# Optimization experiments

Hardware: AMD Instinct MI355X
Metric: run time of the kernel (lower is better)

Reference implementation:

```python
import jax, jax.numpy as jnp
import numpy as np

GROUP_SIZE = 128
EQN = "btd,kdf->btkf"  # x:[B,T,D] @ w:[K,D,F] -> [B,T,K,F]


def setup_inputs() -> dict:
    key = jax.random.key(0)
    k1, k2, k3, k4 = jax.random.split(key, 4)
    B, T, D = 4, 2048, 4096
    K, F = 2, 8192
    G = D // GROUP_SIZE  # 32 quantization groups along D
    x = jax.random.normal(k1, (B, T, D), dtype=jnp.float32)
    qweight = jax.random.randint(k2, (K, D, F), 0, 16, dtype=jnp.int32)  # uint4 values
    qzeros = jax.random.randint(k3, (K, G, F), 0, 16, dtype=jnp.int32)   # uint4 zero points
    scales = jax.random.uniform(k4, (K, G, F), dtype=jnp.float32) * 0.02
    return {"x": x, "qweight": qweight, "qzeros": qzeros, "scales": scales}


def dequantize(imatrix, scales, zeros, group_size, axis_to_repeat):
    rs = jnp.repeat(scales, group_size, axis=axis_to_repeat)
    rz = jnp.repeat(zeros, group_size, axis=axis_to_repeat)
    return (imatrix.astype(rs.dtype) - rz.astype(rs.dtype)) * rs


def reference(x, qweight, qzeros, scales):
    # dequantize int4 weights along axis 1 (hidden/contraction dim), then einsum
    w = dequantize(qweight, scales, qzeros, GROUP_SIZE, axis_to_repeat=1)  # [K,D,F] fp32
    w = w.astype(x.dtype)
    return jnp.einsum(EQN, x, w)  # [B,T,K,F]
```

## Files before the change

kernel.cpp:

```cpp
#include <hip/hip_runtime.h>
#include <hip/hip_bf16.h>
#include <stdint.h>


typedef __attribute__((ext_vector_type(8))) short bf16x8;
typedef __attribute__((ext_vector_type(16))) float f32x16;
typedef __attribute__((ext_vector_type(4))) float f32x4;

static constexpr int Dd = 4096, Ff = 8192;
static constexpr int M = 8192, NTOT = 16384;
static constexpr int NKT2 = Dd / 32;
static constexpr int NMB = M / 256;
static constexpr int NNB = NTOT / 256;

__device__ __forceinline__ short f2bf(float f) {
    __hip_bfloat16 h = __float2bfloat16(f);
    return *reinterpret_cast<short*>(&h);
}

__device__ __forceinline__ int frag_off32(int r, int cb) {
    const int rb = r >> 5, ks = cb >> 1, kh = cb & 1;
    return ((rb * 2 + ks) << 10) + (((r & 31) + 32 * kh) << 4);
}

__global__ __launch_bounds__(256) void xcvt(const float* __restrict__ x,
                                            char* __restrict__ Xw) {
    const int bid = blockIdx.x;
    const int h = bid >> 7, kt2 = bid & 127;
    const int t = threadIdx.x;
    const int r = t >> 1, seg = t & 1;
    const float* src = x + ((size_t)(h * 128 + r)) * Dd + kt2 * 32 + seg * 16;
    char* panel = Xw + ((size_t)bid << 13);
    #pragma unroll
    for (int jj = 0; jj < 2; ++jj) {
        float4 v0 = *reinterpret_cast<const float4*>(src + jj * 8);
        float4 v1 = *reinterpret_cast<const float4*>(src + jj * 8 + 4);
        union { short s[8]; bf16x8 v; } u;
        u.s[0] = f2bf(v0.x); u.s[1] = f2bf(v0.y); u.s[2] = f2bf(v0.z); u.s[3] = f2bf(v0.w);
        u.s[4] = f2bf(v1.x); u.s[5] = f2bf(v1.y); u.s[6] = f2bf(v1.z); u.s[7] = f2bf(v1.w);
        const int cb = seg * 2 + jj;
        *reinterpret_cast<bf16x8*>(panel + frag_off32(r, cb)) = u.v;
    }
}

__global__ __launch_bounds__(256) void wdq(const int* __restrict__ qw,
                                           const int* __restrict__ qz,
                                           const float* __restrict__ sc,
                                           char* __restrict__ Ww) {
    const int bid = blockIdx.x;
    const int fh = bid >> 7, kt2 = bid & 127;
    const int t = threadIdx.x;
    const int r = t & 127, dh = t >> 7;
    const int n = fh * 128 + r;
    const int k = n >> 13, f = n & 8191;
    const int g = kt2 >> 2;
    const int   zv = qz[((size_t)k * 32 + g) * Ff + f];
    const float sv = sc[((size_t)k * 32 + g) * Ff + f];
    const int* qp = qw + ((size_t)(k * Dd + kt2 * 32 + dh * 16)) * Ff + f;
    char* panel = Ww + ((size_t)bid << 13);
    #pragma unroll
    for (int jj = 0; jj < 2; ++jj) {
        union { short s[8]; bf16x8 v; } u;
        #pragma unroll
        for (int e = 0; e < 8; ++e) {
            int q = qp[(size_t)(jj * 8 + e) * Ff];
            u.s[e] = f2bf((float)(q - zv) * sv);
        }
        const int cb = dh * 2 + jj;
        *reinterpret_cast<bf16x8*>(panel + frag_off32(r, cb)) = u.v;
    }
}

#define APAN32(H, KT2) (Xw + (((size_t)(H) * 128 + (KT2)) << 13))
#define BPAN32(H, KT2) (Ww + (((size_t)(H) * 128 + (KT2)) << 13))

#define GLL(GP, LP)                                                                \
    __builtin_amdgcn_global_load_lds(                                              \
        (const __attribute__((address_space(1))) void*)(GP),                       \
        (__attribute__((address_space(3))) void*)(LP), 16, 0, 0)

#define STAGE_TILE(KT2, BUF) do {                                                  \
    GLL(APAN32(bm2,     (KT2)) + woff16, (BUF) +     0 + woffu);                   \
    GLL(APAN32(bm2 + 1, (KT2)) + woff16, (BUF) +  8192 + woffu);                   \
    GLL(BPAN32(bn2,     (KT2)) + woff16, (BUF) + 16384 + woffu);                   \
    GLL(BPAN32(bn2 + 1, (KT2)) + woff16, (BUF) + 24576 + woffu);                   \
} while (0)

#define SB0() __builtin_amdgcn_sched_barrier(0)

#define BODY(KT2, BUFR, DOST, BUFS) do {                                           \
    if (DOST) STAGE_TILE((KT2) + 2, BUFS);                                         \
    bf16x8 a[8], b[4];                                                             \
    _Pragma("unroll")                                                              \
    for (int mb = 0; mb < 4; ++mb)                                                 \
        _Pragma("unroll")                                                          \
        for (int ks = 0; ks < 2; ++ks)                                             \
            a[mb * 2 + ks] = *reinterpret_cast<const bf16x8*>(                     \
                (BUFR) + aoff + (mb * 2 + ks) * 1024);                             \
    _Pragma("unroll")                                                              \
    for (int nf = 0; nf < 2; ++nf)                                                 \
        _Pragma("unroll")                                                          \
        for (int ks = 0; ks < 2; ++ks)                                             \
            b[nf * 2 + ks] = *reinterpret_cast<const bf16x8*>(                     \
                (BUFR) + boff + nf * 2048 + ks * 1024);                            \
    _Pragma("unroll")                                                              \
    for (int ks = 0; ks < 2; ++ks)                                                 \
        _Pragma("unroll")                                                          \
        for (int mb = 0; mb < 4; ++mb)                                             \
            _Pragma("unroll")                                                      \
            for (int nf = 0; nf < 2; ++nf)                                         \
                acc[mb * 2 + nf] = __builtin_amdgcn_mfma_f32_32x32x16_bf16(        \
                    a[mb * 2 + ks], b[nf * 2 + ks], acc[mb * 2 + nf], 0, 0, 0);    \
    if (DOST) asm volatile("s_waitcnt vmcnt(4)" ::: "memory");                     \
    else      asm volatile("s_waitcnt vmcnt(0)" ::: "memory");                     \
    SB0();                                                                         \
    __builtin_amdgcn_s_barrier();                                                  \
    SB0();                                                                         \
} while (0)

__global__ __launch_bounds__(512, 2) void gemm256(const char* __restrict__ Xw,
                                                  const char* __restrict__ Ww,
                                                  float* __restrict__ out) {
    __shared__ char lds[131072];
    char* const L0 = lds;
    char* const L1 = lds + 32768;
    char* const L2 = lds + 65536;
    char* const L3 = lds + 98304;

    const int t = threadIdx.x;
    const int wave = t >> 6, lane = t & 63;
    const int wm = wave >> 2, wn = wave & 3;
    const int l31 = lane & 31;
    const int lane16 = lane << 4;

    const int xcd = blockIdx.x & 7;
    const int c   = blockIdx.x >> 3;
    const int bn  = xcd * 8 + (c >> 5);
    const int bm  = c & 31;
    const int bm2 = bm * 2, bn2 = bn * 2;

    const int woff16 = wave * 1024 + lane16;
    const int woffu  = wave * 1024;
    const int aoff = wm * 8192 + lane16;
    const int boff = 16384 + (wn >> 1) * 8192 + (wn & 1) * 4096 + lane16;

    f32x16 acc[8] = {};

    STAGE_TILE(0, L0);
    STAGE_TILE(1, L1);
    asm volatile("s_waitcnt vmcnt(4)" ::: "memory");
    SB0();
    __builtin_amdgcn_s_barrier();
    SB0();

    for (int i = 0; i < 32; ++i) {
        const int T = i * 4;
        const bool nl = (i < 31);
        BODY(T + 0, L0, true, L2);
        BODY(T + 1, L1, true, L3);
        BODY(T + 2, L2, nl,   L0);
        BODY(T + 3, L3, nl,   L1);
    }

    const int rbase = bm * 256 + wm * 128 + (lane >> 5) * 4;
    const int cbase = bn * 256 + wn * 64 + l31;
    #pragma unroll
    for (int mb = 0; mb < 4; ++mb)
        #pragma unroll
        for (int nf = 0; nf < 2; ++nf)
            #pragma unroll
            for (int reg = 0; reg < 16; ++reg) {
                const int row = rbase + mb * 32 + (reg & 3) + 8 * (reg >> 2);
                __builtin_nontemporal_store(
                    acc[mb * 2 + nf][reg],
                    &out[(size_t)row * NTOT + cbase + nf * 32]);
            }
}

#define LDP 72
__global__ __launch_bounds__(256) void int4_gemm(
    const float* __restrict__ x, const int* __restrict__ qw,
    const int* __restrict__ qz, const float* __restrict__ sc,
    float* __restrict__ out)
{
    __shared__ short As[128][LDP];
    __shared__ short Bs[128][LDP];
    const int t = threadIdx.x;
    int gid = (blockIdx.x & 7) * 1024 + (blockIdx.x >> 3);
    const int bm = gid & 63;
    const int bnq = gid >> 6;
    const int kse = bnq >> 6;
    const int f0  = (bnq & 63) * 128;
    const int m0  = bm * 128;
    const int wave = t >> 6, lane = t & 63;
    const int wm = wave >> 1, wn = wave & 1;
    const int l15 = lane & 15, lhi = lane >> 4;
    const int am = t >> 4, ad = (t & 15) * 4;
    const int bf = t & 127, bd = (t >> 7) * 4;
    const int*   qwk = qw + (size_t)kse * Dd * Ff;
    const int*   qzk = qz + (size_t)kse * 32 * Ff;
    const float* sck = sc + (size_t)kse * 32 * Ff;
    f32x4 acc[4][4] = {};
    for (int d0 = 0; d0 < Dd; d0 += 64) {
        __syncthreads();
        #pragma unroll
        for (int p = 0; p < 8; ++p) {
            int m = p * 16 + am;
            const float4 v = *reinterpret_cast<const float4*>(
                &x[(size_t)(m0 + m) * Dd + d0 + ad]);
            short4 wv;
            wv.x = f2bf(v.x); wv.y = f2bf(v.y); wv.z = f2bf(v.z); wv.w = f2bf(v.w);
            *reinterpret_cast<short4*>(&As[m][ad]) = wv;
        }
        {
            const int g = d0 >> 7;
            const int   zv = qzk[g * Ff + f0 + bf];
            const float sv = sck[g * Ff + f0 + bf];
            #pragma unroll
            for (int p = 0; p < 8; ++p) {
                int dl = p * 8 + bd;
                const int* qp = qwk + (size_t)(d0 + dl) * Ff + f0 + bf;
                short4 wv;
                wv.x = f2bf((float)(qp[0]      - zv) * sv);
                wv.y = f2bf((float)(qp[Ff]     - zv) * sv);
                wv.z = f2bf((float)(qp[2 * Ff] - zv) * sv);
                wv.w = f2bf((float)(qp[3 * Ff] - zv) * sv);
                *reinterpret_cast<short4*>(&Bs[bf][dl]) = wv;
            }
        }
        __syncthreads();
        #pragma unroll
        for (int kk = 0; kk < 64; kk += 32) {
            bf16x8 a2[4], b2[4];
            #pragma unroll
            for (int i = 0; i < 4; ++i)
                a2[i] = *reinterpret_cast<const bf16x8*>(&As[wm * 64 + i * 16 + l15][kk + lhi * 8]);
            #pragma unroll
            for (int i = 0; i < 4; ++i)
                b2[i] = *reinterpret_cast<const bf16x8*>(&Bs[wn * 64 + i * 16 + l15][kk + lhi * 8]);
            #pragma unroll
            for (int mi = 0; mi < 4; ++mi)
                #pragma unroll
                for (int ni = 0; ni < 4; ++ni)
                    acc[mi][ni] = __builtin_amdgcn_mfma_f32_16x16x32_bf16(
                        a2[mi], b2[ni], acc[mi][ni], 0, 0, 0);
        }
    }
    const int crow0 = m0 + wm * 64 + lhi * 4;
    const int ccol0 = bnq * 128 + wn * 64 + l15;
    #pragma unroll
    for (int mi = 0; mi < 4; ++mi)
        #pragma unroll
        for (int ni = 0; ni < 4; ++ni)
            #pragma unroll
            for (int r = 0; r < 4; ++r)
                out[(size_t)(crow0 + mi * 16 + r) * NTOT + ccol0 + ni * 16] =
                    acc[mi][ni][r];
}

extern "C" void kernel_launch(void* const* d_in, const int* in_sizes, int n_in,
                              void* d_out, int out_size, void* d_ws, size_t ws_size,
                              hipStream_t stream) {
    const float* x  = (const float*)d_in[0];
    const int*   qw = (const int*)d_in[1];
    const int*   qz = (const int*)d_in[2];
    const float* sc = (const float*)d_in[3];
    float*       out = (float*)d_out;

    const size_t xw_bytes = (size_t)(M / 128) * NKT2 * 8192;
    const size_t ww_bytes = (size_t)(NTOT / 128) * NKT2 * 8192;

    if (ws_size >= xw_bytes + ww_bytes) {
        char* Xw = (char*)d_ws;
        char* Ww = Xw + xw_bytes;
        hipLaunchKernelGGL(xcvt, dim3((M / 128) * NKT2), dim3(256), 0, stream, x, Xw);
        hipLaunchKernelGGL(wdq, dim3((NTOT / 128) * NKT2), dim3(256), 0, stream,
                           qw, qz, sc, Ww);
        hipLaunchKernelGGL(gemm256, dim3(NMB * NNB), dim3(512), 0, stream,
                           Xw, Ww, out);
    } else {
        hipLaunchKernelGGL(int4_gemm, dim3(8192), dim3(256), 0, stream,
                           x, qw, qz, sc, out);
    }
}
```

Baseline: 1.155 ms.

## Replace 256x256 pipelined GEMM with simpler 128x128 single-buffer tile kernel

New measurement: 1.405 ms. 21.6% more time.

```diff
diff --git a/kernel.cpp b/kernel.cpp
--- a/kernel.cpp
+++ b/kernel.cpp
@@ -10,8 +10,8 @@
 static constexpr int Dd = 4096, Ff = 8192;
 static constexpr int M = 8192, NTOT = 16384;
 static constexpr int NKT2 = Dd / 32;
-static constexpr int NMB = M / 256;
-static constexpr int NNB = NTOT / 256;
+static constexpr int NMB = M / 128;
+static constexpr int NNB = NTOT / 128;
 
 __device__ __forceinline__ short f2bf(float f) {
     __hip_bfloat16 h = __float2bfloat16(f);
@@ -79,101 +79,79 @@
         (const __attribute__((address_space(1))) void*)(GP),                       \
         (__attribute__((address_space(3))) void*)(LP), 16, 0, 0)
 
-#define STAGE_TILE(KT2, BUF) do {                                                  \
-    GLL(APAN32(bm2,     (KT2)) + woff16, (BUF) +     0 + woffu);                   \
-    GLL(APAN32(bm2 + 1, (KT2)) + woff16, (BUF) +  8192 + woffu);                   \
-    GLL(BPAN32(bn2,     (KT2)) + woff16, (BUF) + 16384 + woffu);                   \
-    GLL(BPAN32(bn2 + 1, (KT2)) + woff16, (BUF) + 24576 + woffu);                   \
-} while (0)
-
-#define SB0() __builtin_amdgcn_sched_barrier(0)
-
-#define BODY(KT2, BUFR, DOST, BUFS) do {                                           \
-    if (DOST) STAGE_TILE((KT2) + 2, BUFS);                                         \
-    bf16x8 a[8], b[4];                                                             \
-    _Pragma("unroll")                                                              \
-    for (int mb = 0; mb < 4; ++mb)                                                 \
-        _Pragma("unroll")                                                          \
-        for (int ks = 0; ks < 2; ++ks)                                             \
-            a[mb * 2 + ks] = *reinterpret_cast<const bf16x8*>(                     \
-                (BUFR) + aoff + (mb * 2 + ks) * 1024);                             \
-    _Pragma("unroll")                                                              \
-    for (int nf = 0; nf < 2; ++nf)                                                 \
-        _Pragma("unroll")                                                          \
-        for (int ks = 0; ks < 2; ++ks)                                             \
-            b[nf * 2 + ks] = *reinterpret_cast<const bf16x8*>(                     \
-                (BUFR) + boff + nf * 2048 + ks * 1024);                            \
-    _Pragma("unroll")                                                              \
-    for (int ks = 0; ks < 2; ++ks)                                                 \
-        _Pragma("unroll")                                                          \
-        for (int mb = 0; mb < 4; ++mb)                                             \
-            _Pragma("unroll")                                                      \
-            for (int nf = 0; nf < 2; ++nf)                                         \
-                acc[mb * 2 + nf] = __builtin_amdgcn_mfma_f32_32x32x16_bf16(        \
-                    a[mb * 2 + ks], b[nf * 2 + ks], acc[mb * 2 + nf], 0, 0, 0);    \
-    if (DOST) asm volatile("s_waitcnt vmcnt(4)" ::: "memory");                     \
-    else      asm volatile("s_waitcnt vmcnt(0)" ::: "memory");                     \
-    SB0();                                                                         \
-    __builtin_amdgcn_s_barrier();                                                  \
-    SB0();                                                                         \
-} while (0)
-
-__global__ __launch_bounds__(512, 2) void gemm256(const char* __restrict__ Xw,
+__global__ __launch_bounds__(256, 3) void gemm128(const char* __restrict__ Xw,
                                                   const char* __restrict__ Ww,
                                                   float* __restrict__ out) {
-    __shared__ char lds[131072];
-    char* const L0 = lds;
-    char* const L1 = lds + 32768;
-    char* const L2 = lds + 65536;
-    char* const L3 = lds + 98304;
+    __shared__ char lds[32768];
 
     const int t = threadIdx.x;
     const int wave = t >> 6, lane = t & 63;
-    const int wm = wave >> 2, wn = wave & 3;
-    const int l31 = lane & 31;
+    const int wm = wave >> 1, wn = wave & 1;
     const int lane16 = lane << 4;
 
     const int xcd = blockIdx.x & 7;
     const int c   = blockIdx.x >> 3;
-    const int bn  = xcd * 8 + (c >> 5);
-    const int bm  = c & 31;
-    const int bm2 = bm * 2, bn2 = bn * 2;
+    const int bn  = xcd * 16 + (c >> 6);
+    const int bm  = c & 63;
 
     const int woff16 = wave * 1024 + lane16;
     const int woffu  = wave * 1024;
-    const int aoff = wm * 8192 + lane16;
-    const int boff = 16384 + (wn >> 1) * 8192 + (wn & 1) * 4096 + lane16;
-
-    f32x16 acc[8] = {};
-
-    STAGE_TILE(0, L0);
-    STAGE_TILE(1, L1);
-    asm volatile("s_waitcnt vmcnt(4)" ::: "memory");
-    SB0();
-    __builtin_amdgcn_s_barrier();
-    SB0();
-
-    for (int i = 0; i < 32; ++i) {
-        const int T = i * 4;
-        const bool nl = (i < 31);
-        BODY(T + 0, L0, true, L2);
-        BODY(T + 1, L1, true, L3);
-        BODY(T + 2, L2, nl,   L0);
-        BODY(T + 3, L3, nl,   L1);
-    }
-
-    const int rbase = bm * 256 + wm * 128 + (lane >> 5) * 4;
-    const int cbase = bn * 256 + wn * 64 + l31;
-    #pragma unroll
-    for (int mb = 0; mb < 4; ++mb)
-        #pragma unroll
-        for (int nf = 0; nf < 2; ++nf)
+
+    f32x16 acc[4] = {};
+
+    for (int kt = 0; kt < 64; ++kt) {
+        const char* pa0 = APAN32(bm, 2 * kt);
+        const char* pa1 = APAN32(bm, 2 * kt + 1);
+        const char* pb0 = BPAN32(bn, 2 * kt);
+        const char* pb1 = BPAN32(bn, 2 * kt + 1);
+        GLL(pa0 + woff16,        lds + woffu);
+        GLL(pa0 + 4096 + woff16, lds + 4096 + woffu);
+        GLL(pa1 + woff16,        lds + 8192 + woffu);
+        GLL(pa1 + 4096 + woff16, lds + 12288 + woffu);
+        GLL(pb0 + woff16,        lds + 16384 + woffu);
+        GLL(pb0 + 4096 + woff16, lds + 20480 + woffu);
+        GLL(pb1 + woff16,        lds + 24576 + woffu);
+        GLL(pb1 + 4096 + woff16, lds + 28672 + woffu);
+        __syncthreads();
+
+        #pragma unroll
+        for (int kt2 = 0; kt2 < 2; ++kt2)
+            #pragma unroll
+            for (int ksl = 0; ksl < 2; ++ksl) {
+                bf16x8 af[2], bb[2];
+                #pragma unroll
+                for (int mb = 0; mb < 2; ++mb)
+                    af[mb] = *reinterpret_cast<const bf16x8*>(
+                        lds + kt2 * 8192 +
+                        ((((wm * 2 + mb) * 2) + ksl) << 10) + lane16);
+                #pragma unroll
+                for (int nb = 0; nb < 2; ++nb)
+                    bb[nb] = *reinterpret_cast<const bf16x8*>(
+                        lds + 16384 + kt2 * 8192 +
+                        ((((wn * 2 + nb) * 2) + ksl) << 10) + lane16);
+                #pragma unroll
+                for (int mb = 0; mb < 2; ++mb)
+                    #pragma unroll
+                    for (int nb = 0; nb < 2; ++nb)
+                        acc[mb * 2 + nb] = __builtin_amdgcn_mfma_f32_32x32x16_bf16(
+                            af[mb], bb[nb], acc[mb * 2 + nb], 0, 0, 0);
+            }
+        __syncthreads();
+    }
+
+    const int l31 = lane & 31;
+    const int rbase = bm * 128 + wm * 64 + (lane >> 5) * 4;
+    const int cbase = bn * 128 + wn * 64 + l31;
+    #pragma unroll
+    for (int mb = 0; mb < 2; ++mb)
+        #pragma unroll
+        for (int nb = 0; nb < 2; ++nb)
             #pragma unroll
             for (int reg = 0; reg < 16; ++reg) {
                 const int row = rbase + mb * 32 + (reg & 3) + 8 * (reg >> 2);
                 __builtin_nontemporal_store(
-                    acc[mb * 2 + nf][reg],
-                    &out[(size_t)row * NTOT + cbase + nf * 32]);
+                    acc[mb * 2 + nb][reg],
+                    &out[(size_t)row * NTOT + cbase + nb * 32]);
             }
 }
 
@@ -276,7 +254,7 @@
         hipLaunchKernelGGL(xcvt, dim3((M / 128) * NKT2), dim3(256), 0, stream, x, Xw);
         hipLaunchKernelGGL(wdq, dim3((NTOT / 128) * NKT2), dim3(256), 0, stream,
                            qw, qz, sc, Ww);
-        hipLaunchKernelGGL(gemm256, dim3(NMB * NNB), dim3(512), 0, stream,
+        hipLaunchKernelGGL(gemm128, dim3(NMB * NNB), dim3(256), 0, stream,
                            Xw, Ww, out);
     } else {
         hipLaunchKernelGGL(int4_gemm, dim3(8192), dim3(256), 0, stream,
```
